# Optimization experiments

Measured on AMD Instinct MI355X. Metric: run time of the kernel, lower is better.

## Reference

```python
import jax, jax.numpy as jnp
import numpy as np

B, N = 1, 6            # batch, cameras -> BN = 6
FC, FH, FW = 256, 32, 88
D_ST, D_END, D_STEP = 1.0, 60.0, 1.0
C_OUT = 128
X, Y = 128, 128        # BEV grid
BN_EPS = 1e-3


def setup_inputs() -> dict:
    key = jax.random.key(0)
    ks = jax.random.split(key, 12)
    BNc = B * N
    inp = {
        'relative_depth': jax.random.uniform(ks[0], (BNc, 1, FH, FW), jnp.float32),
        'img_feats': jax.random.normal(ks[1], (BNc, FC, FH, FW), jnp.float32),
        'voxel_ids': jax.random.randint(ks[2], (BNc, 59, FH, FW), 0, X * Y, jnp.int32),
        # aligner + bin converter params (scalars)
        'log_scale': jnp.log(jnp.float32(50.0)),
        'shift': jnp.float32(5.0),
        'log_sigma': jnp.log(jnp.float32(2.0)),
        # feature_net params
        'conv1_w': jax.random.normal(ks[3], (FC, FC, 3, 3), jnp.float32) * 0.02,
        'conv1_b': jnp.zeros((FC,), jnp.float32),
        'bn1_g': jnp.ones((FC,), jnp.float32),
        'bn1_b': jnp.zeros((FC,), jnp.float32),
        'bn1_m': jnp.zeros((FC,), jnp.float32),
        'bn1_v': jnp.ones((FC,), jnp.float32),
        'conv2_w': jax.random.normal(ks[4], (FC, FC, 3, 3), jnp.float32) * 0.02,
        'conv2_b': jnp.zeros((FC,), jnp.float32),
        'bn2_g': jnp.ones((FC,), jnp.float32),
        'bn2_b': jnp.zeros((FC,), jnp.float32),
        'bn2_m': jnp.zeros((FC,), jnp.float32),
        'bn2_v': jnp.ones((FC,), jnp.float32),
        'conv3_w': jax.random.normal(ks[5], (C_OUT, FC, 1, 1), jnp.float32) * 0.02,
        'conv3_b': jnp.zeros((C_OUT,), jnp.float32),
    }
    return inp


def _conv2d(x, w, b, pad):
    y = jax.lax.conv_general_dilated(x, w, (1, 1), [(pad, pad), (pad, pad)],
                                     dimension_numbers=('NCHW', 'OIHW', 'NCHW'))
    return y + b[None, :, None, None]


def _bn_eval(x, g, b, m, v):
    inv = g / jnp.sqrt(v + BN_EPS)
    return (x - m[None, :, None, None]) * inv[None, :, None, None] + b[None, :, None, None]


def reference(relative_depth, img_feats, voxel_ids, log_scale, shift, log_sigma,
              conv1_w, conv1_b, bn1_g, bn1_b, bn1_m, bn1_v,
              conv2_w, conv2_b, bn2_g, bn2_b, bn2_m, bn2_v,
              conv3_w, conv3_b):
    bins = jnp.arange(D_ST, D_END, D_STEP, dtype=jnp.float32)  # (D,) = 59
    D = bins.shape[0]

    # 1) aligner: relative -> metric depth
    metric = jnp.clip(jnp.exp(log_scale) * relative_depth + shift, 0.5, 150.0)  # (BN,1,H,W)

    # 2) Laplace-kernel depth-bin distribution
    sigma = jnp.clip(jnp.exp(log_sigma), 0.1, 20.0)
    logits = -jnp.abs(metric - bins[None, :, None, None]) / sigma  # (BN,D,H,W)
    depth_dist = jax.nn.softmax(logits, axis=1)

    # 3) feature head (convs in eval-mode BN)
    h = jax.nn.relu(_bn_eval(_conv2d(img_feats, conv1_w, conv1_b, 1), bn1_g, bn1_b, bn1_m, bn1_v))
    h = jax.nn.relu(_bn_eval(_conv2d(h, conv2_w, conv2_b, 1), bn2_g, bn2_b, bn2_m, bn2_v))
    feat = _conv2d(h, conv3_w, conv3_b, 0)  # (BN,C,H,W)

    # 4) lift: outer product depth_dist x features -> (BN,C,D,H,W)
    volume = depth_dist[:, None] * feat[:, :, None]

    # 5) splat: scatter-sum frustum points into BEV voxel grid (B,C,X,Y)
    BNc = volume.shape[0]
    pts = jnp.transpose(volume, (0, 2, 3, 4, 1)).reshape(-1, C_OUT)  # (BN*D*H*W, C)
    b_idx = (jnp.arange(BNc, dtype=jnp.int32) // N)[:, None, None, None]
    seg = (b_idx * (X * Y) + voxel_ids).reshape(-1)
    bev = jax.ops.segment_sum(pts, seg, num_segments=B * X * Y)  # (B*X*Y, C)
    bev = jnp.transpose(bev.reshape(B, X, Y, C_OUT), (0, 3, 1, 2))  # (B,C,X,Y)
    return bev
```

## Files before the change

kernel.cpp:

```cpp
#include <hip/hip_runtime.h>
#include <math.h>

#define HW   2816
#define IMGS 6
#define DD   59
#define NV   16384
#define COUT 128
#define NPIX (IMGS*HW)
#define WCUT 1e-5f
#define CAP  128
#define NCONV1 528
#define NFILL  3894

typedef _Float16 half8  __attribute__((ext_vector_type(8)));
typedef _Float16 half2v __attribute__((ext_vector_type(2)));
typedef float f32x4 __attribute__((ext_vector_type(4)));

__device__ __forceinline__ void glds16(const _Float16* g, const _Float16* l){
    __builtin_amdgcn_global_load_lds(
        (const __attribute__((address_space(1))) void*)g,
        (__attribute__((address_space(3))) void*)l, 16, 0, 0);
}


struct DepthCtx { float metric, inv, mx, rs; };

__device__ __forceinline__ DepthCtx depth_ctx(float relv, float lsc, float shf, float lsg){
    DepthCtx c;
    float scale = expf(lsc);
    float sig   = fminf(fmaxf(expf(lsg), 0.1f), 20.f);
    c.inv = 1.f/sig;
    c.metric = fminf(fmaxf(scale*relv + shf, 0.5f), 150.f);
    float nb = fminf(fmaxf(rintf(c.metric), 1.f), 59.f);
    c.mx = -fabsf(c.metric - nb)*c.inv;
    float sum = 0.f;
    for (int d = 0; d < DD; ++d)
        sum += expf(-fabsf(c.metric - (float)(d+1))*c.inv - c.mx);
    c.rs = 1.f/sum;
    return c;
}


__device__ __forceinline__ void wsplit_body(const float* __restrict__ w,
                                            _Float16* __restrict__ wh,
                                            int o, int CO, int CI, int KK){
    if (o >= CO*CI*KK) return;
    int tap = o/(CO*CI);
    int r   = o - tap*CO*CI;
    int co  = r/CI;
    int ci  = r - co*CI;
    wh[o] = (_Float16)w[(co*CI + ci)*KK + tap];
}

__global__ void prep_kernel(int* __restrict__ cursor,
                            const float* __restrict__ w1, _Float16* __restrict__ wh1,
                            const float* __restrict__ w2, _Float16* __restrict__ wh2,
                            const float* __restrict__ w3, _Float16* __restrict__ wh3,
                            const float* __restrict__ c1b, const float* __restrict__ g1,
                            const float* __restrict__ bb1, const float* __restrict__ m1,
                            const float* __restrict__ v1,
                            const float* __restrict__ c2b, const float* __restrict__ g2,
                            const float* __restrict__ bb2, const float* __restrict__ m2,
                            const float* __restrict__ v2,
                            float* __restrict__ s1, float* __restrict__ t1,
                            float* __restrict__ s2, float* __restrict__ t2,
                            const float* __restrict__ rel, const float* __restrict__ lsc,
                            const float* __restrict__ shf, const float* __restrict__ lsg,
                            float4* __restrict__ dparams,
                            const float* __restrict__ imgf, _Float16* __restrict__ inH){
    __shared__ float tile[32][33];
    int b = blockIdx.x, t = threadIdx.x;
    if (b < 65){
        int i = b*256 + t;
        if (i < NV + 64) cursor[i] = 0;
    } else if (b < 2369){
        wsplit_body(w1, wh1, (b-65)*256 + t, 256, 256, 9);
    } else if (b < 4673){
        wsplit_body(w2, wh2, (b-2369)*256 + t, 256, 256, 9);
    } else if (b < 4801){
        wsplit_body(w3, wh3, (b-4673)*256 + t, 128, 256, 1);
    } else if (b == 4801){
        int c = t;
        float i1 = g1[c]/sqrtf(v1[c]+1e-3f);
        s1[c] = i1; t1[c] = (c1b[c]-m1[c])*i1 + bb1[c];
        float i2 = g2[c]/sqrtf(v2[c]+1e-3f);
        s2[c] = i2; t2[c] = (c2b[c]-m2[c])*i2 + bb2[c];
    } else if (b < 4868){
        int g = (b-4802)*256 + t;
        if (g < NPIX){
            DepthCtx c = depth_ctx(rel[g], lsc[0], shf[0], lsg[0]);
            dparams[g] = make_float4(c.metric, c.inv, c.mx, c.rs);
        }
    } else {
        int bb = b - 4868;
        int img = bb/704, rem = bb - img*704;
        int p0 = (rem % 88)*32, c0 = (rem/88)*32;
        int tx = t & 31, ty = t >> 5;
#pragma unroll
        for (int k = 0; k < 4; ++k)
            tile[ty + 8*k][tx] = imgf[((size_t)(img*256 + c0 + ty + 8*k))*HW + p0 + tx];
        __syncthreads();
#pragma unroll
        for (int k = 0; k < 4; ++k)
            inH[((size_t)(img*HW + p0 + ty + 8*k))*256 + c0 + tx] = (_Float16)tile[tx][ty + 8*k];
    }
}

template<int TAPS, bool BN_RELU, int COT>
__device__ __forceinline__ void conv_body(int bx, int by,
    const _Float16* __restrict__ in,
    const _Float16* __restrict__ wT,
    const float* __restrict__ scale, const float* __restrict__ bias,
    _Float16* __restrict__ out,
    const _Float16* __restrict__ zp)
{
    __shared__ __align__(16) _Float16 As[4096];
    __shared__ __align__(16) _Float16 Bs[8192];

    const int t    = threadIdx.x;
    const int wave = t >> 6;
    const int lane = t & 63;
    const int g    = lane >> 4;
    const int l15  = lane & 15;
    const int wr   = wave >> 1, wc = wave & 1;
    const int g0   = bx*64;
    const int img  = g0/HW;
    const int pbase= g0 - img*HW;
    const int n0   = by*128;
    const int imgbase = img*HW;
    const int NK   = TAPS*4;

    int aPy[2], aPx[2], aOct[2], aLo[2];
#pragma unroll
    for (int i = 0; i < 2; ++i){
        int s = i*256 + t;
        int row = s >> 3;
        aOct[i] = ((s & 7) ^ (row & 7))*8;
        int p = pbase + row;
        aPy[i] = p/88; aPx[i] = p - aPy[i]*88;
        aLo[i] = (i*256 + wave*64)*8;
    }
    int bOff[4], bLo[4];
#pragma unroll
    for (int i = 0; i < 4; ++i){
        int s = i*256 + t;
        int row = s >> 3;
        bOff[i] = (n0 + row)*256 + ((s & 7) ^ (row & 7))*8;
        bLo[i]  = (i*256 + wave*64)*8;
    }
    int arow[2], brow[4];
#pragma unroll
    for (int f = 0; f < 2; ++f) arow[f] = wr*32 + f*16 + l15;
#pragma unroll
    for (int f = 0; f < 4; ++f) brow[f] = wc*64 + f*16 + l15;

    f32x4 acc[2][4];
#pragma unroll
    for (int i = 0; i < 2; ++i)
#pragma unroll
        for (int j = 0; j < 4; ++j) acc[i][j] = (f32x4){0.f,0.f,0.f,0.f};

    for (int kk = 0; kk < NK; ++kk){
        const int tap = kk >> 2, ci0 = (kk & 3) << 6;
        const int dy = (TAPS == 9) ? tap/3 - 1 : 0;
        const int dx = (TAPS == 9) ? tap - (tap/3)*3 - 1 : 0;

        __syncthreads();
#pragma unroll
        for (int i = 0; i < 2; ++i){
            int yy = aPy[i] + dy, xx = aPx[i] + dx;
            bool valid = ((unsigned)yy < 32u) && ((unsigned)xx < 88u);
            const _Float16* src = valid
                ? in + (size_t)(imgbase + yy*88 + xx)*256 + ci0 + aOct[i] : zp;
            glds16(src, As + aLo[i]);
        }
        const _Float16* wb = wT + (size_t)tap*COT*256 + ci0;
#pragma unroll
        for (int i = 0; i < 4; ++i)
            glds16(wb + bOff[i], Bs + bLo[i]);
        __syncthreads();

#pragma unroll
        for (int ks = 0; ks < 2; ++ks){
            half8 a[2], bf[4];
#pragma unroll
            for (int f = 0; f < 2; ++f)
                a[f] = *(const half8*)(As + (arow[f]*8 + (((ks*4 + g) ^ (arow[f] & 7))))*8);
#pragma unroll
            for (int f = 0; f < 4; ++f)
                bf[f] = *(const half8*)(Bs + (brow[f]*8 + (((ks*4 + g) ^ (brow[f] & 7))))*8);
#pragma unroll
            for (int mi = 0; mi < 2; ++mi)
#pragma unroll
            for (int ni = 0; ni < 4; ++ni)
                acc[mi][ni] = __builtin_amdgcn_mfma_f32_16x16x32_f16(a[mi], bf[ni], acc[mi][ni], 0,0,0);
        }
    }

#pragma unroll
    for (int ni = 0; ni < 4; ++ni){
        int co = n0 + wc*64 + ni*16 + l15;
        float sc = BN_RELU ? scale[co] : 0.f;
        float bi = bias[co];
#pragma unroll
        for (int mi = 0; mi < 2; ++mi){
            f32x4 v = acc[mi][ni];
            int rb = g0 + wr*32 + mi*16 + g*4;
#pragma unroll
            for (int r = 0; r < 4; ++r){
                float y;
                if (BN_RELU) y = fmaxf(fmaf(v[r], sc, bi), 0.f);
                else         y = v[r] + bi;
                out[(size_t)(rb + r)*COT + co] = (_Float16)y;
            }
        }
    }
}

__device__ __forceinline__ void fill_body(int bb, int t,
    const float4* __restrict__ dparams, const int* __restrict__ vids,
    int* __restrict__ cursor, int2* __restrict__ records){
    int tid = bb*256 + t;
    if (tid >= NPIX*DD) return;
    int d  = tid/NPIX;
    int pp = tid - d*NPIX;
    int bn = pp/HW;
    int p  = pp - bn*HW;
    float4 c = dparams[pp];
    float w = expf(-fabsf(c.x - (float)(d+1))*c.y - c.z)*c.w;
    if (w >= WCUT){
        int v = vids[(bn*DD + d)*HW + p];
        int pos = atomicAdd(&cursor[v], 1);
        if (pos < CAP) records[v*CAP + pos] = make_int2(pp, __float_as_int(w));
    }
}

template<int TAPS, bool BN_RELU, int COT>
__global__ __launch_bounds__(256,6) void conv_mfma(
    const _Float16* __restrict__ in, const _Float16* __restrict__ wT,
    const float* __restrict__ scale, const float* __restrict__ bias,
    _Float16* __restrict__ out, const _Float16* __restrict__ zp){
    conv_body<TAPS,BN_RELU,COT>(blockIdx.x, blockIdx.y, in, wT, scale, bias, out, zp);
}

__global__ __launch_bounds__(256,6) void conv1_fill_kernel(
    const _Float16* __restrict__ in, const _Float16* __restrict__ wT,
    const float* __restrict__ scale, const float* __restrict__ bias,
    _Float16* __restrict__ out, const _Float16* __restrict__ zp,
    const float4* __restrict__ dparams, const int* __restrict__ vids,
    int* __restrict__ cursor, int2* __restrict__ records){
    int b = blockIdx.x;
    if (b < NCONV1){
        conv_body<9,true,256>(b % 264, b / 264, in, wT, scale, bias, out, zp);
    } else {
        fill_body(b - NCONV1, threadIdx.x, dparams, vids, cursor, records);
    }
}

__global__ __launch_bounds__(256,8) void gather_kernel(
    const int2* __restrict__ records, const int* __restrict__ cursor,
    const _Float16* __restrict__ feat16, float* __restrict__ bev_t){
    int v    = blockIdx.x*4 + (threadIdx.x >> 6);
    int lane = threadIdx.x & 63;
    int n = min(cursor[v], CAP);
    const int2* rec = records + v*CAP;
    float a0 = 0.f, a1 = 0.f;
    int i = 0;
    for (; i + 8 <= n; i += 8){
        int2 r[8];
#pragma unroll
        for (int j = 0; j < 8; ++j) r[j] = rec[i+j];
        half2v f[8];
#pragma unroll
        for (int j = 0; j < 8; ++j)
            f[j] = *(const half2v*)(feat16 + (size_t)r[j].x*COUT + lane*2);
#pragma unroll
        for (int j = 0; j < 8; ++j){
            float w = __int_as_float(r[j].y);
            a0 = fmaf(w, (float)f[j][0], a0);
            a1 = fmaf(w, (float)f[j][1], a1);
        }
    }
    for (; i < n; ++i){
        int2 r = rec[i];
        half2v f = *(const half2v*)(feat16 + (size_t)r.x*COUT + lane*2);
        float w = __int_as_float(r.y);
        a0 = fmaf(w, (float)f[0], a0); a1 = fmaf(w, (float)f[1], a1);
    }
    *(float2*)(bev_t + (size_t)v*COUT + lane*2) = make_float2(a0, a1);
}

__global__ void transpose_out(const float* __restrict__ bev_t, float* __restrict__ out){
    __shared__ float tile[32][33];
    int v0 = blockIdx.x*32, c0 = blockIdx.y*32;
    int tx = threadIdx.x & 31, ty = threadIdx.x >> 5;
#pragma unroll
    for (int k = 0; k < 4; ++k)
        tile[ty + 8*k][tx] = bev_t[(size_t)(v0 + ty + 8*k)*COUT + c0 + tx];
    __syncthreads();
#pragma unroll
    for (int k = 0; k < 4; ++k)
        out[(size_t)(c0 + ty + 8*k)*NV + v0 + tx] = tile[tx][ty + 8*k];
}


extern "C" void kernel_launch(void* const* d_in, const int* in_sizes, int n_in,
                              void* d_out, int out_size, void* d_ws, size_t ws_size,
                              hipStream_t stream){
    const float* rel  = (const float*)d_in[0];
    const float* imgf = (const float*)d_in[1];
    const int*   vids = (const int*)d_in[2];
    const float* lsc  = (const float*)d_in[3];
    const float* shf  = (const float*)d_in[4];
    const float* lsg  = (const float*)d_in[5];
    const float* w1   = (const float*)d_in[6];
    const float* b1   = (const float*)d_in[7];
    const float* g1   = (const float*)d_in[8];
    const float* bb1  = (const float*)d_in[9];
    const float* m1   = (const float*)d_in[10];
    const float* v1   = (const float*)d_in[11];
    const float* w2   = (const float*)d_in[12];
    const float* b2   = (const float*)d_in[13];
    const float* g2   = (const float*)d_in[14];
    const float* bb2  = (const float*)d_in[15];
    const float* m2   = (const float*)d_in[16];
    const float* v2   = (const float*)d_in[17];
    const float* w3   = (const float*)d_in[18];
    const float* b3   = (const float*)d_in[19];

    char* ws = (char*)d_ws;
    size_t o = 0;
    auto alloc = [&](size_t bytes)->char*{
        char* p = ws + o;
        o += (bytes + 255) & ~(size_t)255;
        return p;
    };
    int* cursor = (int*)alloc((size_t)(NV + 64)*4);
    const _Float16* zpad16 = (const _Float16*)(cursor + NV);
    float4* dparams = (float4*)alloc((size_t)NPIX*16);

    _Float16* wT1 = (_Float16*)alloc((size_t)9*256*256*2);
    _Float16* wT2 = (_Float16*)alloc((size_t)9*256*256*2);
    _Float16* wT3 = (_Float16*)alloc((size_t)128*256*2);
    float* s1 = (float*)alloc(256*4);
    float* t1 = (float*)alloc(256*4);
    float* s2 = (float*)alloc(256*4);
    float* t2 = (float*)alloc(256*4);

    _Float16* in0 = (_Float16*)alloc((size_t)NPIX*256*2);
    _Float16* h1  = (_Float16*)alloc((size_t)NPIX*256*2);
    _Float16* feat16 = (_Float16*)alloc((size_t)NPIX*COUT*2);
    float* bev_t  = (float*)alloc((size_t)NV*COUT*4);
    int2* records = (int2*)alloc((size_t)NV*CAP*8);
    _Float16* h2 = in0;

    prep_kernel<<<9092,256,0,stream>>>(cursor,
        w1, wT1, w2, wT2, w3, wT3,
        b1,g1,bb1,m1,v1, b2,g2,bb2,m2,v2, s1,t1,s2,t2,
        rel, lsc, shf, lsg, dparams, imgf, in0);

    conv1_fill_kernel<<<NCONV1 + NFILL,256,0,stream>>>(
        in0, wT1, s1, t1, h1, zpad16, dparams, vids, cursor, records);
    conv_mfma<9,true ,256><<<dim3(264,2),256,0,stream>>>(h1,  wT2, s2, t2, h2, zpad16);
    conv_mfma<1,false,128><<<dim3(264,1),256,0,stream>>>(h2,  wT3, s1, b3, feat16, zpad16);

    gather_kernel<<<4096,256,0,stream>>>(records, cursor, feat16, bev_t);
    transpose_out<<<dim3(512,4),256,0,stream>>>(bev_t, (float*)d_out);
}
```

Before: 236.7 us.

## Enlarge conv tiles to 128x128 and vectorize gather with 16-byte feature loads

The conv GEMM tile grows from 64x128 to 128x128 output pixels by channels. Each wave now accumulates 4x4 MFMA fragments, which raises reuse of the weight tile and halves the number of blocks, at the cost of more LDS and registers (launch bounds drop to 4 blocks per SIMD). The gather kernel now has each lane load 8 halves at once, with four lane groups handling interleaved records, and combines the partial sums with cross-lane shuffles. This replaces many small 4-byte loads with wider ones and adds more memory-level parallelism.

Result: slower. 247.5 us (+4.6%).

```diff
diff --git a/kernel.cpp b/kernel.cpp
--- a/kernel.cpp
+++ b/kernel.cpp
@@ -9,11 +9,10 @@
 #define NPIX (IMGS*HW)
 #define WCUT 1e-5f
 #define CAP  128
-#define NCONV1 528
+#define NCONV1 264
 #define NFILL  3894
 
 typedef _Float16 half8  __attribute__((ext_vector_type(8)));
-typedef _Float16 half2v __attribute__((ext_vector_type(2)));
 typedef float f32x4 __attribute__((ext_vector_type(4)));
 
 __device__ __forceinline__ void glds16(const _Float16* g, const _Float16* l){
@@ -114,7 +113,7 @@
     _Float16* __restrict__ out,
     const _Float16* __restrict__ zp)
 {
-    __shared__ __align__(16) _Float16 As[4096];
+    __shared__ __align__(16) _Float16 As[8192];
     __shared__ __align__(16) _Float16 Bs[8192];
 
     const int t    = threadIdx.x;
@@ -123,40 +122,25 @@
     const int g    = lane >> 4;
     const int l15  = lane & 15;
     const int wr   = wave >> 1, wc = wave & 1;
-    const int g0   = bx*64;
+    const int g0   = bx*128;
     const int img  = g0/HW;
     const int pbase= g0 - img*HW;
     const int n0   = by*128;
     const int imgbase = img*HW;
     const int NK   = TAPS*4;
 
-    int aPy[2], aPx[2], aOct[2], aLo[2];
-#pragma unroll
-    for (int i = 0; i < 2; ++i){
-        int s = i*256 + t;
-        int row = s >> 3;
-        aOct[i] = ((s & 7) ^ (row & 7))*8;
-        int p = pbase + row;
-        aPy[i] = p/88; aPx[i] = p - aPy[i]*88;
-        aLo[i] = (i*256 + wave*64)*8;
-    }
-    int bOff[4], bLo[4];
+    int aPy[4], aPx[4];
 #pragma unroll
     for (int i = 0; i < 4; ++i){
         int s = i*256 + t;
         int row = s >> 3;
-        bOff[i] = (n0 + row)*256 + ((s & 7) ^ (row & 7))*8;
-        bLo[i]  = (i*256 + wave*64)*8;
-    }
-    int arow[2], brow[4];
-#pragma unroll
-    for (int f = 0; f < 2; ++f) arow[f] = wr*32 + f*16 + l15;
-#pragma unroll
-    for (int f = 0; f < 4; ++f) brow[f] = wc*64 + f*16 + l15;
-
-    f32x4 acc[2][4];
-#pragma unroll
-    for (int i = 0; i < 2; ++i)
+        int p = pbase + row;
+        aPy[i] = p/88; aPx[i] = p - aPy[i]*88;
+    }
+
+    f32x4 acc[4][4];
+#pragma unroll
+    for (int i = 0; i < 4; ++i)
 #pragma unroll
         for (int j = 0; j < 4; ++j) acc[i][j] = (f32x4){0.f,0.f,0.f,0.f};
 
@@ -166,31 +150,34 @@
         const int dx = (TAPS == 9) ? tap - (tap/3)*3 - 1 : 0;
 
         __syncthreads();
-#pragma unroll
-        for (int i = 0; i < 2; ++i){
+        const _Float16* wb = wT + (size_t)tap*COT*256 + ci0;
+#pragma unroll
+        for (int i = 0; i < 4; ++i){
+            int s   = i*256 + t;
+            int row = s >> 3;
+            int oct = ((s & 7) ^ (row & 7))*8;
+            int lo  = (i*256 + wave*64)*8;
             int yy = aPy[i] + dy, xx = aPx[i] + dx;
             bool valid = ((unsigned)yy < 32u) && ((unsigned)xx < 88u);
-            const _Float16* src = valid
-                ? in + (size_t)(imgbase + yy*88 + xx)*256 + ci0 + aOct[i] : zp;
-            glds16(src, As + aLo[i]);
-        }
-        const _Float16* wb = wT + (size_t)tap*COT*256 + ci0;
-#pragma unroll
-        for (int i = 0; i < 4; ++i)
-            glds16(wb + bOff[i], Bs + bLo[i]);
+            const _Float16* asrc = valid
+                ? in + (size_t)(imgbase + yy*88 + xx)*256 + ci0 + oct : zp;
+            glds16(asrc, As + lo);
+            glds16(wb + (size_t)(n0 + row)*256 + oct, Bs + lo);
+        }
         __syncthreads();
 
 #pragma unroll
         for (int ks = 0; ks < 2; ++ks){
-            half8 a[2], bf[4];
-#pragma unroll
-            for (int f = 0; f < 2; ++f)
-                a[f] = *(const half8*)(As + (arow[f]*8 + (((ks*4 + g) ^ (arow[f] & 7))))*8);
-#pragma unroll
-            for (int f = 0; f < 4; ++f)
-                bf[f] = *(const half8*)(Bs + (brow[f]*8 + (((ks*4 + g) ^ (brow[f] & 7))))*8);
-#pragma unroll
-            for (int mi = 0; mi < 2; ++mi)
+            half8 a[4], bf[4];
+#pragma unroll
+            for (int f = 0; f < 4; ++f){
+                int ar = wr*64 + f*16 + l15;
+                int br = wc*64 + f*16 + l15;
+                a[f]  = *(const half8*)(As + (ar*8 + (((ks*4 + g) ^ (ar & 7))))*8);
+                bf[f] = *(const half8*)(Bs + (br*8 + (((ks*4 + g) ^ (br & 7))))*8);
+            }
+#pragma unroll
+            for (int mi = 0; mi < 4; ++mi)
 #pragma unroll
             for (int ni = 0; ni < 4; ++ni)
                 acc[mi][ni] = __builtin_amdgcn_mfma_f32_16x16x32_f16(a[mi], bf[ni], acc[mi][ni], 0,0,0);
@@ -203,9 +190,9 @@
         float sc = BN_RELU ? scale[co] : 0.f;
         float bi = bias[co];
 #pragma unroll
-        for (int mi = 0; mi < 2; ++mi){
+        for (int mi = 0; mi < 4; ++mi){
             f32x4 v = acc[mi][ni];
-            int rb = g0 + wr*32 + mi*16 + g*4;
+            int rb = g0 + wr*64 + mi*16 + g*4;
 #pragma unroll
             for (int r = 0; r < 4; ++r){
                 float y;
@@ -236,14 +223,14 @@
 }
 
 template<int TAPS, bool BN_RELU, int COT>
-__global__ __launch_bounds__(256,6) void conv_mfma(
+__global__ __launch_bounds__(256,4) void conv_mfma(
     const _Float16* __restrict__ in, const _Float16* __restrict__ wT,
     const float* __restrict__ scale, const float* __restrict__ bias,
     _Float16* __restrict__ out, const _Float16* __restrict__ zp){
     conv_body<TAPS,BN_RELU,COT>(blockIdx.x, blockIdx.y, in, wT, scale, bias, out, zp);
 }
 
-__global__ __launch_bounds__(256,6) void conv1_fill_kernel(
+__global__ __launch_bounds__(256,4) void conv1_fill_kernel(
     const _Float16* __restrict__ in, const _Float16* __restrict__ wT,
     const float* __restrict__ scale, const float* __restrict__ bias,
     _Float16* __restrict__ out, const _Float16* __restrict__ zp,
@@ -251,7 +238,7 @@
     int* __restrict__ cursor, int2* __restrict__ records){
     int b = blockIdx.x;
     if (b < NCONV1){
-        conv_body<9,true,256>(b % 264, b / 264, in, wT, scale, bias, out, zp);
+        conv_body<9,true,256>(b % 132, b / 132, in, wT, scale, bias, out, zp);
     } else {
         fill_body(b - NCONV1, threadIdx.x, dparams, vids, cursor, records);
     }
@@ -262,32 +249,48 @@
     const _Float16* __restrict__ feat16, float* __restrict__ bev_t){
     int v    = blockIdx.x*4 + (threadIdx.x >> 6);
     int lane = threadIdx.x & 63;
+    int q    = lane >> 4;
+    int m    = lane & 15;
     int n = min(cursor[v], CAP);
     const int2* rec = records + v*CAP;
-    float a0 = 0.f, a1 = 0.f;
-    int i = 0;
-    for (; i + 8 <= n; i += 8){
-        int2 r[8];
-#pragma unroll
-        for (int j = 0; j < 8; ++j) r[j] = rec[i+j];
-        half2v f[8];
-#pragma unroll
-        for (int j = 0; j < 8; ++j)
-            f[j] = *(const half2v*)(feat16 + (size_t)r[j].x*COUT + lane*2);
+    float a[8];
+#pragma unroll
+    for (int j = 0; j < 8; ++j) a[j] = 0.f;
+
+    int i = q;
+    for (; i + 12 < n; i += 16){
+        int2 r0 = rec[i], r1 = rec[i+4], r2 = rec[i+8], r3 = rec[i+12];
+        half8 f0 = *(const half8*)(feat16 + (size_t)r0.x*COUT + m*8);
+        half8 f1 = *(const half8*)(feat16 + (size_t)r1.x*COUT + m*8);
+        half8 f2 = *(const half8*)(feat16 + (size_t)r2.x*COUT + m*8);
+        half8 f3 = *(const half8*)(feat16 + (size_t)r3.x*COUT + m*8);
+        float w0 = __int_as_float(r0.y), w1 = __int_as_float(r1.y);
+        float w2 = __int_as_float(r2.y), w3 = __int_as_float(r3.y);
 #pragma unroll
         for (int j = 0; j < 8; ++j){
-            float w = __int_as_float(r[j].y);
-            a0 = fmaf(w, (float)f[j][0], a0);
-            a1 = fmaf(w, (float)f[j][1], a1);
-        }
-    }
-    for (; i < n; ++i){
+            a[j] = fmaf(w0, (float)f0[j], a[j]);
+            a[j] = fmaf(w1, (float)f1[j], a[j]);
+            a[j] = fmaf(w2, (float)f2[j], a[j]);
+            a[j] = fmaf(w3, (float)f3[j], a[j]);
+        }
+    }
+    for (; i < n; i += 4){
         int2 r = rec[i];
-        half2v f = *(const half2v*)(feat16 + (size_t)r.x*COUT + lane*2);
+        half8 f = *(const half8*)(feat16 + (size_t)r.x*COUT + m*8);
         float w = __int_as_float(r.y);
-        a0 = fmaf(w, (float)f[0], a0); a1 = fmaf(w, (float)f[1], a1);
-    }
-    *(float2*)(bev_t + (size_t)v*COUT + lane*2) = make_float2(a0, a1);
+#pragma unroll
+        for (int j = 0; j < 8; ++j) a[j] = fmaf(w, (float)f[j], a[j]);
+    }
+#pragma unroll
+    for (int j = 0; j < 8; ++j){
+        a[j] += __shfl_xor(a[j], 16);
+        a[j] += __shfl_xor(a[j], 32);
+    }
+    if (q == 0){
+        float* o = bev_t + (size_t)v*COUT + m*8;
+        *(float4*)(o)     = make_float4(a[0], a[1], a[2], a[3]);
+        *(float4*)(o + 4) = make_float4(a[4], a[5], a[6], a[7]);
+    }
 }
 
 __global__ void transpose_out(const float* __restrict__ bev_t, float* __restrict__ out){
@@ -361,8 +364,8 @@
 
     conv1_fill_kernel<<<NCONV1 + NFILL,256,0,stream>>>(
         in0, wT1, s1, t1, h1, zpad16, dparams, vids, cursor, records);
-    conv_mfma<9,true ,256><<<dim3(264,2),256,0,stream>>>(h1,  wT2, s2, t2, h2, zpad16);
-    conv_mfma<1,false,128><<<dim3(264,1),256,0,stream>>>(h2,  wT3, s1, b3, feat16, zpad16);
+    conv_mfma<9,true ,256><<<dim3(132,2),256,0,stream>>>(h1,  wT2, s2, t2, h2, zpad16);
+    conv_mfma<1,false,128><<<dim3(132,1),256,0,stream>>>(h2,  wT3, s1, b3, feat16, zpad16);
 
     gather_kernel<<<4096,256,0,stream>>>(records, cursor, feat16, bev_t);
     transpose_out<<<dim3(512,4),256,0,stream>>>(bev_t, (float*)d_out);
```
